# Performance work log

Measured on AMD Instinct MI355X. Metric: run time of the kernel, lower is better.

## Reference

```python
import jax, jax.numpy as jnp
import numpy as np

N_NODES = 10000


def _gcn_norm(edge_index, edge_weight, n):
    # PyG GCNConv default: add self-loops (weight 1), symmetric normalization.
    ar = jnp.arange(n, dtype=edge_index.dtype)
    ei = jnp.concatenate([edge_index, jnp.stack([ar, ar])], axis=1)
    ew = jnp.concatenate([edge_weight, jnp.ones((n,), edge_weight.dtype)], axis=0)
    row, col = ei[0], ei[1]
    deg = jax.ops.segment_sum(ew, col, num_segments=n)
    dis = jnp.where(deg > 0, jax.lax.rsqrt(jnp.where(deg > 0, deg, 1.0)), 0.0)
    norm = dis[row] * ew * dis[col]
    return row, col, norm


def _gcn_conv(h, W, b, row, col, norm, n):
    hw = h @ W                                    # [N, out]
    msg = norm[:, None] * hw[row]                 # gather + edge scale
    return jax.ops.segment_sum(msg, col, num_segments=n) + b


def setup_inputs() -> dict:
    key = jax.random.key(0)
    ks = jax.random.split(key, 8)
    N, E, D, H1, H2 = N_NODES, 160000, 256, 128, 64
    return {
        "x": jax.random.normal(ks[0], (N, D), jnp.float32),
        "edge_index": jax.random.randint(ks[1], (2, E), 0, N, jnp.int64 if jax.config.jax_enable_x64 else jnp.int32),
        "edge_weight": jax.random.uniform(ks[2], (E,), jnp.float32),
        "noise": jax.random.normal(ks[3], (N, H2), jnp.float32),
        "W1": jax.random.normal(ks[4], (D, H1), jnp.float32) * (1.0 / np.sqrt(D)),
        "b1": jnp.zeros((H1,), jnp.float32),
        "W2": jax.random.normal(ks[5], (H1, H2), jnp.float32) * (1.0 / np.sqrt(H1)),
        "b2": jnp.zeros((H2,), jnp.float32),
        "W3": jax.random.normal(ks[6], (H1, H2), jnp.float32) * (1.0 / np.sqrt(H1)),
        "b3": jnp.zeros((H2,), jnp.float32),
    }


def reference(x, edge_index, edge_weight, noise, W1, b1, W2, b2, W3, b3):
    n = x.shape[0]
    row, col, norm = _gcn_norm(edge_index, edge_weight, n)
    h = jax.nn.relu(_gcn_conv(x, W1, b1, row, col, norm, n))
    mean = _gcn_conv(h, W2, b2, row, col, norm, n)
    log_std = _gcn_conv(h, W3, b3, row, col, norm, n)
    z = mean + noise * jnp.exp(log_std)           # reparameterization
    adj_rec = jax.nn.sigmoid(z @ z.T)             # [N, N] dot-product decode
    return adj_rec
```

## Files before the change

### kernel.cpp

```cpp
#include <hip/hip_runtime.h>


#define Nn 10000
#define Np 10112
#define NpK (Np * 64)

typedef short short8 __attribute__((ext_vector_type(8)));
typedef float f32x4 __attribute__((ext_vector_type(4)));
typedef unsigned short ushort4e __attribute__((ext_vector_type(4)));

static __device__ __forceinline__ float sigmoidf(float v) {
  return __builtin_amdgcn_rcpf(1.0f + __expf(-v));
}
static __device__ __forceinline__ unsigned short f32_to_bf16(float f) {
  unsigned int u = __float_as_uint(f);
  unsigned int r = (u + 0x7FFF + ((u >> 16) & 1)) >> 16;
  return (unsigned short)r;
}
static __device__ __forceinline__ float bf16_to_f32(unsigned short s) {
  return __uint_as_float(((unsigned int)s) << 16);
}

__global__ void k_init(float* __restrict__ deg, int* __restrict__ cnt, int n,
                       unsigned short* __restrict__ zh, unsigned short* __restrict__ zl) {
  int i = blockIdx.x * 256 + threadIdx.x;
  if (i < n) { deg[i] = 1.0f; cnt[i] = 0; }
  if (i < (Np - Nn) * 64) { zh[Nn * 64 + i] = 0; zl[Nn * 64 + i] = 0; }
}

__global__ void k_edge_pre(const int* __restrict__ col, const float* __restrict__ ew,
                           float* __restrict__ deg, int* __restrict__ cnt, int E) {
  int e = blockIdx.x * 256 + threadIdx.x;
  if (e < E) { int c = col[e]; atomicAdd(&deg[c], ew[e]); atomicAdd(&cnt[c], 1); }
}

__global__ void k_dis(float* __restrict__ deg, int n) {
  int i = blockIdx.x * 256 + threadIdx.x;
  if (i < n) { float d = deg[i]; deg[i] = (d > 0.0f) ? rsqrtf(d) : 0.0f; }
}

__global__ __launch_bounds__(256) void k_scan(const int* __restrict__ cnt,
                                              int* __restrict__ ofs, int* __restrict__ ofs2,
                                              int n) {
  __shared__ int partial[256];
  const int t = threadIdx.x;
  const int CH = (n + 255) / 256;
  const int start = t * CH;
  int local = 0;
  for (int j = 0; j < CH; ++j) {
    int idx = start + j;
    if (idx < n) local += cnt[idx];
  }
  partial[t] = local;
  __syncthreads();
  for (int off = 1; off < 256; off <<= 1) {
    int x = (t >= off) ? partial[t - off] : 0;
    __syncthreads();
    partial[t] += x;
    __syncthreads();
  }
  int run = partial[t] - local;
  for (int j = 0; j < CH; ++j) {
    int idx = start + j;
    if (idx < n) {
      ofs[idx] = run; ofs2[idx] = run;
      run += cnt[idx];
    }
  }
  if (t == 255) { ofs[n] = run; ofs2[n] = run; }
}

__global__ void k_fill(const int* __restrict__ row, const int* __restrict__ col,
                       const float* __restrict__ ew, const float* __restrict__ dis,
                       int* __restrict__ ofs2, int* __restrict__ csr_src,
                       float* __restrict__ csr_w, int E) {
  int e = blockIdx.x * 256 + threadIdx.x;
  if (e < E) {
    int r = row[e], c = col[e];
    int p = atomicAdd(&ofs2[c], 1);
    csr_src[p] = r;
    csr_w[p] = dis[r] * ew[e] * dis[c];
  }
}

__global__ __launch_bounds__(256) void k_gemm1(const float* __restrict__ x,
                                               const float* __restrict__ W1,
                                               float* __restrict__ hw1) {
  __shared__ float xs[16][68];
  __shared__ float ws[64][128];
  const int tid = threadIdx.x;
  const int row0 = blockIdx.x * 16;
  const int j0 = (tid & 31) * 4;
  const int r0 = (tid >> 5) * 2;
  const int lr = tid >> 4, lk = tid & 15;
  float acc0[4] = {0, 0, 0, 0}, acc1[4] = {0, 0, 0, 0};
  for (int k0 = 0; k0 < 256; k0 += 64) {
    *(float4*)&xs[lr][lk * 4] = *(const float4*)&x[(row0 + lr) * 256 + k0 + lk * 4];
#pragma unroll
    for (int it = 0; it < 8; ++it) {
      int idx4 = tid + it * 256;
      int kk = idx4 >> 5, jq = idx4 & 31;
      *(float4*)&ws[kk][jq * 4] = *(const float4*)&W1[(k0 + kk) * 128 + jq * 4];
    }
    __syncthreads();
#pragma unroll 8
    for (int kk = 0; kk < 64; ++kk) {
      float a0 = xs[r0][kk], a1 = xs[r0 + 1][kk];
      float4 w = *(const float4*)&ws[kk][j0];
      acc0[0] += a0 * w.x; acc0[1] += a0 * w.y; acc0[2] += a0 * w.z; acc0[3] += a0 * w.w;
      acc1[0] += a1 * w.x; acc1[1] += a1 * w.y; acc1[2] += a1 * w.z; acc1[3] += a1 * w.w;
    }
    __syncthreads();
  }
  *(float4*)&hw1[(row0 + r0) * 128 + j0] = make_float4(acc0[0], acc0[1], acc0[2], acc0[3]);
  *(float4*)&hw1[(row0 + r0 + 1) * 128 + j0] = make_float4(acc1[0], acc1[1], acc1[2], acc1[3]);
}

__global__ __launch_bounds__(256) void k_agg(const int* __restrict__ ofs,
                                             const int* __restrict__ csr_src,
                                             const float* __restrict__ csr_w,
                                             const float* __restrict__ feat,
                                             const float* __restrict__ dis,
                                             const float* __restrict__ b,
                                             float* __restrict__ out, int n, int relu_in) {
  int node = blockIdx.x * 4 + (threadIdx.x >> 6);
  if (node >= n) return;
  int f2 = threadIdx.x & 63;
  const float2* featv = (const float2*)feat;
  int s = ofs[node], e = ofs[node + 1];
  float d = dis[node];
  float2 self = featv[node * 64 + f2];
  float2 acc;
  if (relu_in) {
    acc.x = d * d * fmaxf(self.x, 0.0f);
    acc.y = d * d * fmaxf(self.y, 0.0f);
  } else {
    float2 bb = ((const float2*)b)[f2];
    acc.x = d * d * self.x + bb.x;
    acc.y = d * d * self.y + bb.y;
  }
  for (int j = s; j < e; ++j) {
    int r = csr_src[j];
    float wt = csr_w[j];
    float2 v = featv[r * 64 + f2];
    if (relu_in) { v.x = fmaxf(v.x, 0.0f); v.y = fmaxf(v.y, 0.0f); }
    acc.x += wt * v.x;
    acc.y += wt * v.y;
  }
  ((float2*)out)[node * 64 + f2] = acc;
}

__global__ __launch_bounds__(256) void k_gemm2z(const float* __restrict__ hagg,
                                                const float* __restrict__ W2, const float* __restrict__ W3,
                                                const float* __restrict__ b2, const float* __restrict__ b3,
                                                const float* __restrict__ noise,
                                                unsigned short* __restrict__ zh,
                                                unsigned short* __restrict__ zl) {
  __shared__ float xs[16][68];
  __shared__ float ws[64][128];
  __shared__ float zs[16][128];
  const int tid = threadIdx.x;
  const int row0 = blockIdx.x * 16;
  const int j0 = (tid & 31) * 4;
  const int r0 = (tid >> 5) * 2;
  const int lr = tid >> 4, lk = tid & 15;
  float acc0[4] = {0, 0, 0, 0}, acc1[4] = {0, 0, 0, 0};
  for (int k0 = 0; k0 < 128; k0 += 64) {
    *(float4*)&xs[lr][lk * 4] = *(const float4*)&hagg[(row0 + lr) * 128 + k0 + lk * 4];
#pragma unroll
    for (int it = 0; it < 8; ++it) {
      int idx4 = tid + it * 256;
      int kk = idx4 >> 5, jq = idx4 & 31;
      int j = jq * 4;
      float4 wv;
      if (j < 64) wv = *(const float4*)&W2[(k0 + kk) * 64 + j];
      else        wv = *(const float4*)&W3[(k0 + kk) * 64 + (j - 64)];
      *(float4*)&ws[kk][j] = wv;
    }
    __syncthreads();
#pragma unroll 8
    for (int kk = 0; kk < 64; ++kk) {
      float a0 = xs[r0][kk], a1 = xs[r0 + 1][kk];
      float4 w = *(const float4*)&ws[kk][j0];
      acc0[0] += a0 * w.x; acc0[1] += a0 * w.y; acc0[2] += a0 * w.z; acc0[3] += a0 * w.w;
      acc1[0] += a1 * w.x; acc1[1] += a1 * w.y; acc1[2] += a1 * w.z; acc1[3] += a1 * w.w;
    }
    __syncthreads();
  }
  {
    float4 bb = (j0 < 64) ? *(const float4*)&b2[j0] : *(const float4*)&b3[j0 - 64];
    zs[r0][j0 + 0] = acc0[0] + bb.x; zs[r0][j0 + 1] = acc0[1] + bb.y;
    zs[r0][j0 + 2] = acc0[2] + bb.z; zs[r0][j0 + 3] = acc0[3] + bb.w;
    zs[r0 + 1][j0 + 0] = acc1[0] + bb.x; zs[r0 + 1][j0 + 1] = acc1[1] + bb.y;
    zs[r0 + 1][j0 + 2] = acc1[2] + bb.z; zs[r0 + 1][j0 + 3] = acc1[3] + bb.w;
  }
  __syncthreads();
  {
    const int r = tid >> 4;
    const int jj = (tid & 15) * 4;
    float4 mn = *(const float4*)&zs[r][jj];
    float4 ls = *(const float4*)&zs[r][64 + jj];
    float4 nz = *(const float4*)&noise[(row0 + r) * 64 + jj];
    float z0 = mn.x + nz.x * __expf(ls.x);
    float z1 = mn.y + nz.y * __expf(ls.y);
    float z2 = mn.z + nz.z * __expf(ls.z);
    float z3 = mn.w + nz.w * __expf(ls.w);
    ushort4e h, l;
    h[0] = f32_to_bf16(z0); l[0] = f32_to_bf16(z0 - bf16_to_f32(h[0]));
    h[1] = f32_to_bf16(z1); l[1] = f32_to_bf16(z1 - bf16_to_f32(h[1]));
    h[2] = f32_to_bf16(z2); l[2] = f32_to_bf16(z2 - bf16_to_f32(h[2]));
    h[3] = f32_to_bf16(z3); l[3] = f32_to_bf16(z3 - bf16_to_f32(h[3]));
    *(ushort4e*)&zh[(row0 + r) * 64 + jj] = h;
    *(ushort4e*)&zl[(row0 + r) * 64 + jj] = l;
  }
}

__global__ __launch_bounds__(256) void k_decode(const unsigned short* __restrict__ zh,
                                                const unsigned short* __restrict__ zl,
                                                float* __restrict__ out, int n) {
  const int tid = threadIdx.x;
  const int wave = tid >> 6, lane = tid & 63;
  const int rows0 = blockIdx.y * 128 + (wave >> 1) * 64;
  const int cols0 = blockIdx.x * 128 + (wave & 1) * 64;
  const int lrow = lane & 15;
  const int quad = lane >> 4;
  f32x4 acc[4][4];
#pragma unroll
  for (int m = 0; m < 4; ++m)
#pragma unroll
    for (int nn = 0; nn < 4; ++nn) acc[m][nn] = (f32x4){0.0f, 0.0f, 0.0f, 0.0f};

#pragma unroll
  for (int kc = 0; kc < 64; kc += 32) {
    const int ko = kc + quad * 8;
    short8 rh[4], rl[4], ch[4], cl[4];
#pragma unroll
    for (int m = 0; m < 4; ++m) {
      rh[m] = *(const short8*)&zh[(rows0 + m * 16 + lrow) * 64 + ko];
      rl[m] = *(const short8*)&zl[(rows0 + m * 16 + lrow) * 64 + ko];
    }
#pragma unroll
    for (int nn = 0; nn < 4; ++nn) {
      ch[nn] = *(const short8*)&zh[(cols0 + nn * 16 + lrow) * 64 + ko];
      cl[nn] = *(const short8*)&zl[(cols0 + nn * 16 + lrow) * 64 + ko];
    }
#pragma unroll
    for (int m = 0; m < 4; ++m)
#pragma unroll
      for (int nn = 0; nn < 4; ++nn) {
        acc[m][nn] = __builtin_amdgcn_mfma_f32_16x16x32_bf16(ch[nn], rh[m], acc[m][nn], 0, 0, 0);
        acc[m][nn] = __builtin_amdgcn_mfma_f32_16x16x32_bf16(cl[nn], rh[m], acc[m][nn], 0, 0, 0);
        acc[m][nn] = __builtin_amdgcn_mfma_f32_16x16x32_bf16(ch[nn], rl[m], acc[m][nn], 0, 0, 0);
      }
  }

#pragma unroll
  for (int m = 0; m < 4; ++m) {
    int gr = rows0 + m * 16 + lrow;
    if (gr >= n) continue;
#pragma unroll
    for (int nn = 0; nn < 4; ++nn) {
      int c0 = cols0 + nn * 16 + quad * 4;
      if (c0 >= n) continue;
      f32x4 v;
      v[0] = sigmoidf(acc[m][nn][0]);
      v[1] = sigmoidf(acc[m][nn][1]);
      v[2] = sigmoidf(acc[m][nn][2]);
      v[3] = sigmoidf(acc[m][nn][3]);
      __builtin_nontemporal_store(v, (f32x4*)&out[(size_t)gr * n + c0]);
    }
  }
}

extern "C" void kernel_launch(void* const* d_in, const int* in_sizes, int n_in,
                              void* d_out, int out_size, void* d_ws, size_t ws_size,
                              hipStream_t stream) {
  const float* x     = (const float*)d_in[0];
  const int*   ei    = (const int*)d_in[1];
  const float* ew    = (const float*)d_in[2];
  const float* noise = (const float*)d_in[3];
  const float* W1    = (const float*)d_in[4];
  const float* b1    = (const float*)d_in[5];
  const float* W2    = (const float*)d_in[6];
  const float* b2    = (const float*)d_in[7];
  const float* W3    = (const float*)d_in[8];
  const float* b3    = (const float*)d_in[9];
  const int E = in_sizes[2];
  const int n = Nn;
  const int* row = ei;
  const int* col = ei + E;

  float* dis = (float*)d_ws;
  unsigned short* zh = (unsigned short*)((char*)d_ws + 10240 * 4);
  unsigned short* zl = zh + NpK;

  float* S    = (float*)d_out;
  float* hw1  = S;
  float* h    = S + 1310720;
  float* hagg = S + 2621440;
  float* csr_w  = S + 5242880;
  int* csr_src  = (int*)(S + 5402880);
  int* ofs      = (int*)(S + 5562880);
  int* ofs2     = (int*)(S + 5572896);
  int* cnt      = (int*)(S + 5582912);

  k_init<<<(n + 255) / 256, 256, 0, stream>>>(dis, cnt, n, zh, zl);
  k_edge_pre<<<(E + 255) / 256, 256, 0, stream>>>(col, ew, dis, cnt, E);
  k_dis<<<(n + 255) / 256, 256, 0, stream>>>(dis, n);
  k_scan<<<1, 256, 0, stream>>>(cnt, ofs, ofs2, n);
  k_fill<<<(E + 255) / 256, 256, 0, stream>>>(row, col, ew, dis, ofs2, csr_src, csr_w, E);

  k_gemm1<<<n / 16, 256, 0, stream>>>(x, W1, hw1);
  k_agg<<<(n + 3) / 4, 256, 0, stream>>>(ofs, csr_src, csr_w, hw1, dis, b1, h, n, 0);
  k_agg<<<(n + 3) / 4, 256, 0, stream>>>(ofs, csr_src, csr_w, h, dis, b1, hagg, n, 1);

  k_gemm2z<<<n / 16, 256, 0, stream>>>(hagg, W2, W3, b2, b3, noise, zh, zl);

  dim3 g((n + 127) / 128, (n + 127) / 128);
  k_decode<<<g, 256, 0, stream>>>(zh, zl, (float*)d_out, n);
}
```

Baseline: 605.5 us.

## Stage decode z tiles in swizzled LDS, unroll aggregation, move ReLU to output

The decode kernel now cooperatively loads the 128-row and 128-column bf16 hi/lo tiles of z into XOR-swizzled shared memory once per block, instead of each wave loading its operands directly from global memory. The output stores become regular stores rather than nontemporal stores. The aggregation kernel unrolls its edge loop by two and applies bias plus ReLU to its output, so the following pass no longer applies ReLU to each gathered neighbour. The LDS staging adds 64 KB of shared memory per block, which may limit occupancy, and the host-side mode arguments must match the new meaning.

```diff
diff --git a/kernel.cpp b/kernel.cpp
--- a/kernel.cpp
+++ b/kernel.cpp
@@ -122,7 +122,7 @@
                                              const float* __restrict__ feat,
                                              const float* __restrict__ dis,
                                              const float* __restrict__ b,
-                                             float* __restrict__ out, int n, int relu_in) {
+                                             float* __restrict__ out, int n, int mode) {
   int node = blockIdx.x * 4 + (threadIdx.x >> 6);
   if (node >= n) return;
   int f2 = threadIdx.x & 63;
@@ -130,24 +130,32 @@
   int s = ofs[node], e = ofs[node + 1];
   float d = dis[node];
   float2 self = featv[node * 64 + f2];
-  float2 acc;
-  if (relu_in) {
-    acc.x = d * d * fmaxf(self.x, 0.0f);
-    acc.y = d * d * fmaxf(self.y, 0.0f);
+  float accx = d * d * self.x, accy = d * d * self.y;
+  int j = s;
+  for (; j + 2 <= e; j += 2) {
+    int r0 = csr_src[j], r1 = csr_src[j + 1];
+    float w0 = csr_w[j], w1 = csr_w[j + 1];
+    float2 v0 = featv[r0 * 64 + f2];
+    float2 v1 = featv[r1 * 64 + f2];
+    accx += w0 * v0.x + w1 * v1.x;
+    accy += w0 * v0.y + w1 * v1.y;
+  }
+  if (j < e) {
+    int r0 = csr_src[j];
+    float w0 = csr_w[j];
+    float2 v0 = featv[r0 * 64 + f2];
+    accx += w0 * v0.x;
+    accy += w0 * v0.y;
+  }
+  float2 o;
+  if (mode == 0) {
+    float2 bb = ((const float2*)b)[f2];
+    o.x = fmaxf(accx + bb.x, 0.0f);
+    o.y = fmaxf(accy + bb.y, 0.0f);
   } else {
-    float2 bb = ((const float2*)b)[f2];
-    acc.x = d * d * self.x + bb.x;
-    acc.y = d * d * self.y + bb.y;
-  }
-  for (int j = s; j < e; ++j) {
-    int r = csr_src[j];
-    float wt = csr_w[j];
-    float2 v = featv[r * 64 + f2];
-    if (relu_in) { v.x = fmaxf(v.x, 0.0f); v.y = fmaxf(v.y, 0.0f); }
-    acc.x += wt * v.x;
-    acc.y += wt * v.y;
-  }
-  ((float2*)out)[node * 64 + f2] = acc;
+    o.x = accx; o.y = accy;
+  }
+  ((float2*)out)[node * 64 + f2] = o;
 }
 
 __global__ __launch_bounds__(256) void k_gemm2z(const float* __restrict__ hagg,
@@ -218,10 +226,35 @@
 __global__ __launch_bounds__(256) void k_decode(const unsigned short* __restrict__ zh,
                                                 const unsigned short* __restrict__ zl,
                                                 float* __restrict__ out, int n) {
+  __shared__ short zhr[128][64];
+  __shared__ short zlr[128][64];
+  __shared__ short zhc[128][64];
+  __shared__ short zlc[128][64];
   const int tid = threadIdx.x;
+  const int R0 = blockIdx.y * 128;
+  const int C0 = blockIdx.x * 128;
+
+  {
+    const int seg = tid & 7;
+#pragma unroll
+    for (int p = 0; p < 4; ++p) {
+      const int rr = (p << 5) + (tid >> 3);
+      const int sw = (seg ^ (rr & 7)) * 8;
+      short8 vhr = *(const short8*)&zh[(size_t)(R0 + rr) * 64 + seg * 8];
+      short8 vlr = *(const short8*)&zl[(size_t)(R0 + rr) * 64 + seg * 8];
+      short8 vhc = *(const short8*)&zh[(size_t)(C0 + rr) * 64 + seg * 8];
+      short8 vlc = *(const short8*)&zl[(size_t)(C0 + rr) * 64 + seg * 8];
+      *(short8*)&zhr[rr][sw] = vhr;
+      *(short8*)&zlr[rr][sw] = vlr;
+      *(short8*)&zhc[rr][sw] = vhc;
+      *(short8*)&zlc[rr][sw] = vlc;
+    }
+  }
+  __syncthreads();
+
   const int wave = tid >> 6, lane = tid & 63;
-  const int rows0 = blockIdx.y * 128 + (wave >> 1) * 64;
-  const int cols0 = blockIdx.x * 128 + (wave & 1) * 64;
+  const int lr0 = (wave >> 1) * 64;
+  const int lc0 = (wave & 1) * 64;
   const int lrow = lane & 15;
   const int quad = lane >> 4;
   f32x4 acc[4][4];
@@ -232,17 +265,21 @@
 
 #pragma unroll
   for (int kc = 0; kc < 64; kc += 32) {
-    const int ko = kc + quad * 8;
+    const int cb = (kc >> 3) + quad;
     short8 rh[4], rl[4], ch[4], cl[4];
 #pragma unroll
     for (int m = 0; m < 4; ++m) {
-      rh[m] = *(const short8*)&zh[(rows0 + m * 16 + lrow) * 64 + ko];
-      rl[m] = *(const short8*)&zl[(rows0 + m * 16 + lrow) * 64 + ko];
+      int row = lr0 + m * 16 + lrow;
+      int sw = (cb ^ (row & 7)) * 8;
+      rh[m] = *(const short8*)&zhr[row][sw];
+      rl[m] = *(const short8*)&zlr[row][sw];
     }
 #pragma unroll
     for (int nn = 0; nn < 4; ++nn) {
-      ch[nn] = *(const short8*)&zh[(cols0 + nn * 16 + lrow) * 64 + ko];
-      cl[nn] = *(const short8*)&zl[(cols0 + nn * 16 + lrow) * 64 + ko];
+      int row = lc0 + nn * 16 + lrow;
+      int sw = (cb ^ (row & 7)) * 8;
+      ch[nn] = *(const short8*)&zhc[row][sw];
+      cl[nn] = *(const short8*)&zlc[row][sw];
     }
 #pragma unroll
     for (int m = 0; m < 4; ++m)
@@ -256,18 +293,18 @@
 
 #pragma unroll
   for (int m = 0; m < 4; ++m) {
-    int gr = rows0 + m * 16 + lrow;
+    int gr = R0 + lr0 + m * 16 + lrow;
     if (gr >= n) continue;
 #pragma unroll
     for (int nn = 0; nn < 4; ++nn) {
-      int c0 = cols0 + nn * 16 + quad * 4;
+      int c0 = C0 + lc0 + nn * 16 + quad * 4;
       if (c0 >= n) continue;
       f32x4 v;
       v[0] = sigmoidf(acc[m][nn][0]);
       v[1] = sigmoidf(acc[m][nn][1]);
       v[2] = sigmoidf(acc[m][nn][2]);
       v[3] = sigmoidf(acc[m][nn][3]);
-      __builtin_nontemporal_store(v, (f32x4*)&out[(size_t)gr * n + c0]);
+      *(f32x4*)&out[(size_t)gr * n + c0] = v;
     }
   }
 }
```

After: 575.4 us. 1.05x faster.
